# Performance work log

Measured on AMD Instinct MI355X. Metric: run time of the kernel, lower is better.

## Reference

```python
import jax, jax.numpy as jnp
from jax import lax
import numpy as np

NE = 8          # ne_num
IDX_REF = 4     # ne_num // 2
EPS_BN = 1e-5


def conv2d(x, w, b=None, pad=0):
    out = lax.conv_general_dilated(x, w, (1, 1), [(pad, pad), (pad, pad)],
                                   dimension_numbers=('NCHW', 'OIHW', 'NCHW'))
    if b is not None:
        out = out + b[None, :, None, None]
    return out


def bn(x, gamma, beta):
    # training-mode batch norm (biased variance), as nn.BatchNorm2d in train()
    mu = x.mean(axis=(0, 2, 3), keepdims=True)
    var = x.var(axis=(0, 2, 3), keepdims=True)
    xn = (x - mu) * lax.rsqrt(var + EPS_BN)
    return xn * gamma[None, :, None, None] + beta[None, :, None, None]


def gauss_win(sigma):
    # sigma: (B,1). window_size=3 -> bias = [-1, 0, -1]; pop center of 3x3 -> (B,8)
    bias = jnp.array([-1.0, 0.0, -1.0], dtype=sigma.dtype)
    g = jnp.exp(bias[None, :] / (2.0 * sigma ** 2))            # (B,3)
    w1 = g / g.sum(axis=1, keepdims=True)                      # (B,3)
    w2 = (w1[:, :, None] * w1[:, None, :]).reshape(-1, 9)      # (B,9)
    return jnp.concatenate([w2[:, :4], w2[:, 5:]], axis=1)     # (B,8) center removed


def bilinear(img, y, x):
    # img: (B,H,W); y,x: (B,K,H,W) float sample coords; zero padding outside
    B, H, W = img.shape
    y0 = jnp.floor(y); x0 = jnp.floor(x)
    wy1 = y - y0; wy0 = 1.0 - wy1
    wx1 = x - x0; wx0 = 1.0 - wx1
    imgf = img.reshape(B, -1)

    def gather(yi, xi):
        yii = yi.astype(jnp.int32); xii = xi.astype(jnp.int32)
        valid = (yii >= 0) & (yii < H) & (xii >= 0) & (xii < W)
        idx = jnp.clip(yii, 0, H - 1) * W + jnp.clip(xii, 0, W - 1)
        v = jnp.take_along_axis(imgf, idx.reshape(B, -1), axis=1).reshape(idx.shape)
        return jnp.where(valid, v, 0.0)

    return (wy0 * wx0 * gather(y0, x0) + wy0 * wx1 * gather(y0, x0 + 1.0)
            + wy1 * wx0 * gather(y0 + 1.0, x0) + wy1 * wx1 * gather(y0 + 1.0, x0 + 1.0))


def modulated_deform_conv_1x9(fusion, offset, mask):
    # ModulatedDeformConvFunction with weight=ones(1,1,3,3), bias=0, stride=1,
    # pad=1, dilation=1, groups=1, deformable_groups=1.
    # fusion: (B,1,H,W); offset: (B,9,2,H,W) [per-neighbor (dy,dx)]; mask: (B,9,H,W)
    B, _, H, W = fusion.shape
    k = jnp.arange(9)
    py = (k // 3 - 1).astype(fusion.dtype)[None, :, None, None]
    px = (k % 3 - 1).astype(fusion.dtype)[None, :, None, None]
    hh = jnp.arange(H, dtype=fusion.dtype)[None, None, :, None]
    ww = jnp.arange(W, dtype=fusion.dtype)[None, None, None, :]
    y = hh + py + offset[:, :, 0]
    x = ww + px + offset[:, :, 1]
    samp = bilinear(fusion[:, 0], y, x)            # (B,9,H,W)
    return (mask * samp).sum(axis=1, keepdims=True)  # (B,1,H,W)


def _forward(feat, g1_w, g1_g, g1_b, g2_w, g2_g, g2_b, g3_w, g3_bias,
             f1_w, f1_g, f1_b, f2_w, f2_bias,
             s1_w, s1_b, s2_w, s2_b, s3_w, s3_b,
             oa1_w, oa1_g, oa1_b, oa2_w, oa2_g, oa2_b, oa3_w, oa3_bias,
             aff_scale):
    B, _, H, W = feat.shape
    # guid branch (5x5 convs)
    guid = jax.nn.relu(bn(conv2d(feat, g1_w, pad=2), g1_g, g1_b))
    guid = jax.nn.relu(bn(conv2d(guid, g2_w, pad=2), g2_g, g2_b))
    guid = conv2d(guid, g3_w, g3_bias, pad=2)                      # (B,8,H,W)
    # fuse branch
    f = jax.nn.relu(bn(conv2d(feat, f1_w, pad=1), f1_g, f1_b))
    fusion = jnp.tanh(conv2d(f, f2_w, f2_bias, pad=1))             # (B,1,H,W)
    # sigma branch (CAM, detached input)
    fd = lax.stop_gradient(feat)
    p = fd.mean(axis=(2, 3))                                       # (B,32)
    h = jax.nn.celu(p @ s1_w.T + s1_b)
    h = jax.nn.celu(h @ s2_w.T + s2_b)
    sigma = jax.nn.relu(h @ s3_w.T + s3_b) + 0.001                 # (B,1)
    # get_off_aff(guid, sigma, sigma_gamma=0.2, window_size=3)
    oa = jax.nn.relu(bn(conv2d(guid, oa1_w, pad=2), oa1_g, oa1_b))
    oa = jax.nn.relu(bn(conv2d(oa, oa2_w, pad=2), oa2_g, oa2_b))
    oa = conv2d(oa, oa3_w, oa3_bias, pad=2)                        # (B,24,H,W)
    o1, o2, affc = jnp.split(oa, 3, axis=1)                        # each (B,8,H,W)
    off = jnp.concatenate([o1, o2], axis=1).reshape(B, NE, 2, H, W)
    zero_ref = jnp.zeros((B, 1, 2, H, W), dtype=off.dtype)
    offset = jnp.concatenate([off[:, :IDX_REF], zero_ref, off[:, IDX_REF:]], axis=1)  # (B,9,2,H,W)
    gk = gauss_win(sigma + 0.2)                                    # (B,8)
    aff = jnp.tanh(affc) / (aff_scale + 1e-5) + gk[:, :, None, None]
    sa = jnp.abs(aff).sum(axis=1, keepdims=True) + 1e-5
    sa = jnp.maximum(sa, 1.0)
    aff = aff / sa
    aff_ref = 1.0 - aff.sum(axis=1, keepdims=True)
    aff9 = jnp.concatenate([aff[:, :IDX_REF], aff_ref, aff[:, IDX_REF:]], axis=1)  # (B,9,H,W)
    # gauss_filter (times=1) + abs
    gfusion = jnp.abs(modulated_deform_conv_1x9(fusion, offset, aff9))
    return gfusion


def setup_inputs() -> dict:
    key = jax.random.key(0)
    ks = list(jax.random.split(key, 32))
    B, C, H, W = 8, 32, 320, 320
    ne = NE
    d = {}
    d['feat'] = jax.random.normal(ks[0], (B, C, H, W), jnp.float32)

    def wconv(k, o, i, s):
        return jax.random.normal(k, (o, i, s, s), jnp.float32) * (1.0 / np.sqrt(i * s * s))

    def wlin(k, o, i):
        return jax.random.normal(k, (o, i), jnp.float32) * (1.0 / np.sqrt(i))

    # guid: 32->32 (5), 32->8 (5), 8->8 (5, bias)
    d['g1_w'] = wconv(ks[1], C, C, 5); d['g1_g'] = jnp.ones(C) + 0.1 * jax.random.normal(ks[2], (C,)); d['g1_b'] = 0.1 * jax.random.normal(ks[3], (C,))
    d['g2_w'] = wconv(ks[4], ne, C, 5); d['g2_g'] = jnp.ones(ne) + 0.1 * jax.random.normal(ks[5], (ne,)); d['g2_b'] = 0.1 * jax.random.normal(ks[6], (ne,))
    d['g3_w'] = wconv(ks[7], ne, ne, 5); d['g3_bias'] = 0.1 * jax.random.normal(ks[8], (ne,))
    # fuse: 32->32 (3), 32->1 (3, bias)
    d['f1_w'] = wconv(ks[9], C, C, 3); d['f1_g'] = jnp.ones(C) + 0.1 * jax.random.normal(ks[10], (C,)); d['f1_b'] = 0.1 * jax.random.normal(ks[11], (C,))
    d['f2_w'] = wconv(ks[12], 1, C, 3); d['f2_bias'] = 0.1 * jax.random.normal(ks[13], (1,))
    # gen_sigma CAM: 32->16->16->1
    d['s1_w'] = wlin(ks[14], 16, C); d['s1_b'] = 0.1 * jax.random.normal(ks[15], (16,))
    d['s2_w'] = wlin(ks[16], 16, 16); d['s2_b'] = 0.1 * jax.random.normal(ks[17], (16,))
    d['s3_w'] = wlin(ks[18], 1, 16); d['s3_b'] = 0.1 * jax.random.normal(ks[19], (1,))
    # conv_off_aff: 8->8 (5), 8->24 (5), 24->24 (5, bias)
    d['oa1_w'] = wconv(ks[20], ne, ne, 5); d['oa1_g'] = jnp.ones(ne) + 0.1 * jax.random.normal(ks[21], (ne,)); d['oa1_b'] = 0.1 * jax.random.normal(ks[22], (ne,))
    d['oa2_w'] = wconv(ks[23], 3 * ne, ne, 5); d['oa2_g'] = jnp.ones(3 * ne) + 0.1 * jax.random.normal(ks[24], (3 * ne,)); d['oa2_b'] = 0.1 * jax.random.normal(ks[25], (3 * ne,))
    d['oa3_w'] = wconv(ks[26], 3 * ne, 3 * ne, 5); d['oa3_bias'] = 0.1 * jax.random.normal(ks[27], (3 * ne,))
    # aff_scale_const = aff_gamma * ne_num = 0.5 * 8
    d['aff_scale'] = jnp.full((1,), 4.0, jnp.float32)
    return d


def reference(feat, g1_w, g1_g, g1_b, g2_w, g2_g, g2_b, g3_w, g3_bias,
              f1_w, f1_g, f1_b, f2_w, f2_bias,
              s1_w, s1_b, s2_w, s2_b, s3_w, s3_b,
              oa1_w, oa1_g, oa1_b, oa2_w, oa2_g, oa2_b, oa3_w, oa3_bias,
              aff_scale):
    return _forward(feat, g1_w, g1_g, g1_b, g2_w, g2_g, g2_b, g3_w, g3_bias,
                    f1_w, f1_g, f1_b, f2_w, f2_bias,
                    s1_w, s1_b, s2_w, s2_b, s3_w, s3_b,
                    oa1_w, oa1_g, oa1_b, oa2_w, oa2_g, oa2_b, oa3_w, oa3_bias,
                    aff_scale)
```

## Files before the change

### kernel.cpp

```cpp
#include <hip/hip_runtime.h>
#include <hip/hip_bf16.h>
#include <math.h>

#define B_   8
#define H_   320
#define W_   320
#define HW_  (320*320)

typedef __attribute__((ext_vector_type(8))) short bf16x8;
typedef __attribute__((ext_vector_type(4))) short bf16x4s;
typedef __attribute__((ext_vector_type(4))) float f32x4;

__device__ __forceinline__ short f2b(float v){
    __hip_bfloat16 h = __float2bfloat16(v);
    return *(short*)&h;
}
__device__ __forceinline__ float bf2f(short v){
    unsigned u = ((unsigned)(unsigned short)v) << 16;
    return __uint_as_float(u);
}

__global__ void convert_k(const float* __restrict__ in, short* __restrict__ out,
                          float* __restrict__ psum){
    const int b  = blockIdx.y;
    const int px = blockIdx.x*256 + threadIdx.x;
    const float* src = in + (long)b*32*HW_ + px;
    short* dst = out + ((long)b*HW_ + px)*32;
    float f[32];
    short v[32];
    #pragma unroll
    for (int c=0;c<32;++c){ f[c] = src[(long)c*HW_]; v[c] = f2b(f[c]); }
    #pragma unroll
    for (int s=0;s<4;++s)
        *(bf16x8*)(dst + s*8) = *(bf16x8*)(v + s*8);
    #pragma unroll
    for (int c=0;c<32;++c){
        float s = f[c];
        #pragma unroll
        for (int o=1;o<64;o<<=1) s += __shfl_xor(s, o, 64);
        f[c] = s;
    }
    __shared__ float red[4][32];
    const int lane = threadIdx.x & 63, wid = threadIdx.x >> 6;
    if (lane < 32) red[wid][lane] = f[lane];
    __syncthreads();
    if (threadIdx.x < 32)
        atomicAdd(&psum[b*32 + threadIdx.x],
                  red[0][threadIdx.x]+red[1][threadIdx.x]+red[2][threadIdx.x]+red[3][threadIdx.x]);
}

__global__ void repack_k(const float* __restrict__ sf1, const float* __restrict__ sf2,
                         const float* __restrict__ sg1, const float* __restrict__ sg2,
                         const float* __restrict__ sg3, const float* __restrict__ so1,
                         const float* __restrict__ so2, const float* __restrict__ so3,
                         short* __restrict__ dst){
    const int cum[8]  = {9216,13824,39424,52224,55808,59392,66560,92160};
    const int CINs[8] = {32,32,32,32, 8, 8, 8,24};
    const int CIps[8] = {32,32,32,32, 8, 8, 8,32};
    const int COUTs[8]= {32, 1,32, 8, 8, 8,24,24};
    const int MTs[8]  = { 2, 1, 2, 1, 1, 1, 2, 2};
    const int Ks[8]   = { 3, 3, 5, 5, 5, 5, 5, 5};
    int i = blockIdx.x*256 + threadIdx.x;
    if (i >= 92160) return;
    int s = 0;
    while (i >= cum[s]) ++s;
    const int base = s ? cum[s-1] : 0;
    const int il = i - base;
    const float* src = (s==0)?sf1:(s==1)?sf2:(s==2)?sg1:(s==3)?sg2:(s==4)?sg3:(s==5)?so1:(s==6)?so2:so3;
    const int kl   = il & 31;
    const int co_l = (il >> 5) & 15;
    const int rem  = il >> 9;
    const int MT = MTs[s];
    const int mt = rem % MT;
    const int c  = rem / MT;
    const int K = Ks[s];
    int tap, ci;
    if (CIps[s] == 32){ tap = (c % K)*K + (c / K); ci = kl; }
    else              { tap = c*4 + (kl>>3); ci = kl & 7; }
    const int co = mt*16 + co_l;
    float v = 0.f;
    if (co < COUTs[s] && ci < CINs[s] && tap < K*K){
        const int ky = tap / K, kx = tap - ky*K;
        v = src[((co*CINs[s] + ci)*K + ky)*K + kx];
    }
    dst[i] = f2b(v);
}

__device__ __forceinline__
float deform_px(const float* val, const float* __restrict__ fus_b,
                const float* __restrict__ gk_b, float inv_s, int y, int x){
    float aff[8]; float sa = 0.f;
    #pragma unroll
    for (int n=0;n<8;++n){
        float a = tanhf(val[16+n]) * inv_s + gk_b[n];
        aff[n] = a; sa += fabsf(a);
    }
    sa += 1e-5f;
    sa = fmaxf(sa, 1.f);
    const float isa = 1.f/sa;
    float ssum = 0.f;
    #pragma unroll
    for (int n=0;n<8;++n){ aff[n] *= isa; ssum += aff[n]; }
    const float aff_ref = 1.f - ssum;

    float o = 0.f;
    #pragma unroll
    for (int k=0;k<9;++k){
        float dy, dx, m;
        if (k == 4){ dy = 0.f; dx = 0.f; m = aff_ref; }
        else {
            const int n = (k < 4) ? k : k-1;
            dy = val[2*n];
            dx = val[2*n+1];
            m  = aff[n];
        }
        float yy = (float)(y + k/3 - 1) + dy;
        float xx = (float)(x + k%3 - 1) + dx;
        float y0f = floorf(yy), x0f = floorf(xx);
        int   y0 = (int)y0f,    x0i = (int)x0f;
        float wy1 = yy - y0f, wy0 = 1.f - wy1;
        float wx1 = xx - x0f, wx0 = 1.f - wx1;
        float v00 = (y0  >=0 && y0  <H_ && x0i  >=0 && x0i  <W_) ? fus_b[ y0   *W_ + x0i  ] : 0.f;
        float v01 = (y0  >=0 && y0  <H_ && x0i+1>=0 && x0i+1<W_) ? fus_b[ y0   *W_ + x0i+1] : 0.f;
        float v10 = (y0+1>=0 && y0+1<H_ && x0i  >=0 && x0i  <W_) ? fus_b[(y0+1)*W_ + x0i  ] : 0.f;
        float v11 = (y0+1>=0 && y0+1<H_ && x0i+1>=0 && x0i+1<W_) ? fus_b[(y0+1)*W_ + x0i+1] : 0.f;
        o += m * (wy0*(wx0*v00 + wx1*v01) + wy1*(wx0*v10 + wx1*v11));
    }
    return fabsf(o);
}

template<int CIN, int CIp, int COUT, int MT, int K,
         bool IN_BN, bool OUT_STATS, int OUT_MODE, int OCP>
__global__ __launch_bounds__(256, 4)
void mconv_k(const void* __restrict__ inv,
             const float* __restrict__ bn_sum, const float* __restrict__ bn_sq,
             const float* __restrict__ gamma, const float* __restrict__ beta,
             const short* __restrict__ wr, const float* __restrict__ bias,
             void* __restrict__ outv,
             float* __restrict__ osum, float* __restrict__ osq,
             const float* __restrict__ fus, const float* __restrict__ gk,
             const float* __restrict__ aff_scale){
    constexpr int PAD = K/2;
    constexpr int TH  = 8;
    constexpr int LW  = 32 + K - 1;
    constexpr int LH  = TH + K - 1;
    constexpr int SEGS = CIp/8;
    constexpr int PLANE = LH*LW*8 + 8;
    constexpr int NTAPS  = K*K;
    constexpr int NCHUNK = (CIp==32) ? NTAPS : (NTAPS*CIp + 31)/32;
    constexpr int INB  = (CIp==32) ? (SEGS*PLANE*2) : (LH*LW*8*2);
    constexpr int DUMPB = 256*25*4;
    constexpr int LDSB = (OUT_MODE==3 && INB < DUMPB) ? DUMPB : INB;

    __shared__ __align__(16) char ldsraw[LDSB];
    short* lds_in = (short*)ldsraw;
    __shared__ float sc_sh[2][32];
    __shared__ float red[2][4][32];

    const int tid = threadIdx.x;
    const int b   = blockIdx.z;
    const int x0  = blockIdx.x*32, y0 = blockIdx.y*TH;

    const int lane = tid & 63;
    const int wv   = tid >> 6;
    const int pxn  = lane & 15;
    const int quad = lane >> 4;
    const int row0 = 2*wv;

    if (IN_BN){
        if (tid < 32){
            float s = 1.f, sh2 = 0.f;
            if (tid < CIN){
                const float invN = 1.f/(float)(B_*HW_);
                float mu  = bn_sum[tid]*invN;
                float var = bn_sq[tid]*invN - mu*mu;
                s   = gamma[tid] * rsqrtf(var + 1e-5f);
                sh2 = beta[tid] - mu*s;
            }
            sc_sh[0][tid] = s;
            sc_sh[1][tid] = sh2;
        }
        __syncthreads();
    }

    constexpr int KC = (CIp==32) ? K : 1;
    bf16x8 aC[KC][MT];
    bf16x8 aAll[(CIp==8)?NCHUNK:1][MT];

    if constexpr (CIp == 32){
        #pragma unroll
        for (int ky=0; ky<K; ++ky)
            #pragma unroll
            for (int m=0;m<MT;++m)
                aC[ky][m] = *(const bf16x8*)(wr + ((ky*MT + m)*16 + pxn)*32 + quad*8);
    } else {
        #pragma unroll
        for (int c=0;c<NCHUNK;++c)
            #pragma unroll
            for (int m=0;m<MT;++m)
                aAll[c][m] = *(const bf16x8*)(wr + (((c*MT + m)*16 + pxn)*32 + quad*8));
    }

    {
        const short* src = (const short*)inv + (long)b*HW_*CIp;
        constexpr int NU = LH*LW*SEGS;
        constexpr int NIT = (NU + 255)/256;
        bf16x8 vv[NIT];
        int    la[NIT];
        bool   ib[NIT];
        #pragma unroll
        for (int it=0; it<NIT; ++it){
            const int u = tid + it*256;
            bf16x8 v = {0,0,0,0,0,0,0,0};
            bool inb = false;
            int addr = 0;
            if (u < NU){
                const int r   = u / (LW*SEGS);
                const int rem = u - r*(LW*SEGS);
                const int xl  = rem / SEGS;
                const int seg = rem - xl*SEGS;
                const int gy = y0 + r - PAD, gx = x0 + xl - PAD;
                addr = seg*PLANE + (r*LW + xl)*8;
                inb = (gy>=0 && gy<H_ && gx>=0 && gx<W_);
                if (inb)
                    v = *(const bf16x8*)(src + ((long)gy*W_ + gx)*CIp + seg*8);
            }
            vv[it] = v; la[it] = addr; ib[it] = inb;
        }
        __builtin_amdgcn_sched_barrier(0);
        #pragma unroll
        for (int it=0; it<NIT; ++it){
            const int u = tid + it*256;
            if (u < NU){
                bf16x8 v = vv[it];
                if (IN_BN && ib[it]){
                    const int seg = u - (u/SEGS)*SEGS;
                    #pragma unroll
                    for (int j=0;j<8;++j){
                        float f = bf2f(v[j]);
                        f = fmaxf(fmaf(f, sc_sh[0][seg*8+j], sc_sh[1][seg*8+j]), 0.f);
                        v[j] = f2b(f);
                    }
                }
                *(bf16x8*)&lds_in[la[it]] = v;
            }
        }
    }
    __syncthreads();

    const f32x4 zero = {0.f, 0.f, 0.f, 0.f};
    f32x4 acc[2][MT][2];
    #pragma unroll
    for (int rr=0;rr<2;++rr)
        #pragma unroll
        for (int m=0;m<MT;++m){ acc[rr][m][0] = zero; acc[rr][m][1] = zero; }

    if constexpr (CIp == 32){
        const short* bbase = lds_in + quad*PLANE + (row0*LW + pxn)*8;
        #pragma unroll
        for (int kx=0; kx<K; ++kx){
            bf16x8 bw[3][2];
            #pragma unroll
            for (int r=0;r<2;++r)
                #pragma unroll
                for (int n=0;n<2;++n)
                    bw[r][n] = *(const bf16x8*)(bbase + (r*LW + kx + n*16)*8);
            __builtin_amdgcn_sched_barrier(0);
            #pragma unroll
            for (int ky=0; ky<K; ++ky){
                if (ky < K-1){
                    #pragma unroll
                    for (int n=0;n<2;++n)
                        bw[(ky+2)%3][n] = *(const bf16x8*)(bbase + ((ky+2)*LW + kx + n*16)*8);
                }
                __builtin_amdgcn_sched_barrier(0);
                #pragma unroll
                for (int m=0;m<MT;++m){
                    acc[0][m][0] = __builtin_amdgcn_mfma_f32_16x16x32_bf16(aC[ky][m], bw[ky%3][0],     acc[0][m][0], 0,0,0);
                    acc[0][m][1] = __builtin_amdgcn_mfma_f32_16x16x32_bf16(aC[ky][m], bw[ky%3][1],     acc[0][m][1], 0,0,0);
                    acc[1][m][0] = __builtin_amdgcn_mfma_f32_16x16x32_bf16(aC[ky][m], bw[(ky+1)%3][0], acc[1][m][0], 0,0,0);
                    acc[1][m][1] = __builtin_amdgcn_mfma_f32_16x16x32_bf16(aC[ky][m], bw[(ky+1)%3][1], acc[1][m][1], 0,0,0);
                }
                if (kx+1 < K){
                    #pragma unroll
                    for (int m=0;m<MT;++m)
                        aC[ky][m] = *(const bf16x8*)(wr + ((((kx+1)*K+ky)*MT + m)*16 + pxn)*32 + quad*8);
                }
            }
        }
    } else {
        auto bptr = [&](int c, int rr)->const short*{
            const int row = row0 + rr;
            int t = c*4 + quad;
            if (t >= NTAPS) t = 0;
            const int ky = t / K, kx = t - ky*K;
            return lds_in + ((row+ky)*LW + kx + pxn)*8;
        };

        bf16x8 bcp[2][2][2];
        #pragma unroll
        for (int rr=0;rr<2;++rr){
            const short* bp = bptr(0, rr);
            bcp[0][rr][0] = *(const bf16x8*)bp;
            bcp[0][rr][1] = *(const bf16x8*)(bp + 16*8);
        }

        #pragma unroll
        for (int c=0; c<NCHUNK; ++c){
            if (c+1 < NCHUNK){
                #pragma unroll
                for (int rr=0;rr<2;++rr){
                    const short* bpn = bptr(c+1, rr);
                    bcp[(c+1)&1][rr][0] = *(const bf16x8*)bpn;
                    bcp[(c+1)&1][rr][1] = *(const bf16x8*)(bpn + 16*8);
                }
            }
            __builtin_amdgcn_sched_barrier(0);
            #pragma unroll
            for (int m=0;m<MT;++m)
                #pragma unroll
                for (int rr=0;rr<2;++rr){
                    acc[rr][m][0] = __builtin_amdgcn_mfma_f32_16x16x32_bf16(aAll[c][m], bcp[c&1][rr][0], acc[rr][m][0], 0,0,0);
                    acc[rr][m][1] = __builtin_amdgcn_mfma_f32_16x16x32_bf16(aAll[c][m], bcp[c&1][rr][1], acc[rr][m][1], 0,0,0);
                }
        }
    }

    if (OUT_STATS){
        #pragma unroll
        for (int m=0;m<MT;++m){
            #pragma unroll
            for (int r=0;r<4;++r){
                float v  = acc[0][m][0][r] + acc[0][m][1][r]
                         + acc[1][m][0][r] + acc[1][m][1][r];
                float v2 = acc[0][m][0][r]*acc[0][m][0][r] + acc[0][m][1][r]*acc[0][m][1][r]
                         + acc[1][m][0][r]*acc[1][m][0][r] + acc[1][m][1][r]*acc[1][m][1][r];
                #pragma unroll
                for (int o=1;o<16;o<<=1){
                    v  += __shfl_xor(v,  o, 64);
                    v2 += __shfl_xor(v2, o, 64);
                }
                if (pxn == 0){
                    red[0][wv][m*16 + quad*4 + r] = v;
                    red[1][wv][m*16 + quad*4 + r] = v2;
                }
            }
        }
        __syncthreads();
        if (tid < MT*16 && tid < COUT){
            atomicAdd(&osum[tid], red[0][0][tid]+red[0][1][tid]+red[0][2][tid]+red[0][3][tid]);
            atomicAdd(&osq[tid],  red[1][0][tid]+red[1][1][tid]+red[1][2][tid]+red[1][3][tid]);
        }
    }

    if (OUT_MODE == 3){
        float* out = (float*)outv;
        __syncthreads();
        float* dumpf = (float*)ldsraw;
        #pragma unroll
        for (int rr=0;rr<2;++rr){
            const int row = row0 + rr;
            #pragma unroll
            for (int m=0;m<MT;++m){
                if (m*16 + quad*4 < 24){
                    #pragma unroll
                    for (int n=0;n<2;++n)
                        #pragma unroll
                        for (int r=0;r<4;++r)
                            dumpf[(row*32 + n*16 + pxn)*25 + (m*16 + quad*4 + r)] = acc[rr][m][n][r];
                }
            }
        }
        __syncthreads();
        {
            float val[24];
            #pragma unroll
            for (int c2=0;c2<24;++c2) val[c2] = dumpf[tid*25 + c2] + bias[c2];
            const int yy = y0 + (tid>>5), xx = x0 + (tid&31);
            const float inv_s = 1.f/(aff_scale[0] + 1e-5f);
            out[(long)b*HW_ + yy*W_ + xx] =
                deform_px(val, fus + (long)b*HW_, gk + b*8, inv_s, yy, xx);
        }
    } else if (OUT_MODE == 2){
        float* out = (float*)outv;
        #pragma unroll
        for (int rr=0;rr<2;++rr){
            const int y = y0 + row0 + rr;
            #pragma unroll
            for (int m=0;m<MT;++m){
                #pragma unroll
                for (int r=0;r<4;++r){
                    const int co = m*16 + quad*4 + r;
                    if (co < COUT){
                        float* op = out + (((long)b*COUT + co)*H_ + y)*W_ + x0;
                        #pragma unroll
                        for (int n=0;n<2;++n)
                            op[n*16 + pxn] = tanhf(acc[rr][m][n][r] + bias[co]);
                    }
                }
            }
        }
    } else {
        short* o = (short*)outv;
        #pragma unroll
        for (int rr=0;rr<2;++rr){
            const int y = y0 + row0 + rr;
            #pragma unroll
            for (int m=0;m<MT;++m){
                const int co0 = m*16 + quad*4;
                if (co0 < OCP){
                    #pragma unroll
                    for (int n=0;n<2;++n){
                        bf16x4s pk;
                        #pragma unroll
                        for (int r=0;r<4;++r){
                            float f = acc[rr][m][n][r];
                            if (OUT_MODE == 1) f += bias[co0+r];
                            pk[r] = f2b(f);
                        }
                        const long px = ((long)b*H_ + y)*W_ + x0 + n*16 + pxn;
                        *(bf16x4s*)(o + px*OCP + co0) = pk;
                    }
                }
            }
        }
    }
}

__global__ void sigma_k(const float* __restrict__ p,
                        const float* s1w, const float* s1b,
                        const float* s2w, const float* s2b,
                        const float* s3w, const float* s3b,
                        float* __restrict__ gk){
    const int b = threadIdx.x;
    if (b >= B_) return;
    float pb[32];
    for (int j=0;j<32;++j) pb[j] = p[b*32+j] * (1.f/(float)HW_);
    float h1[16], h2[16];
    for (int i=0;i<16;++i){
        float t = s1b[i];
        for (int j=0;j<32;++j) t = fmaf(pb[j], s1w[i*32+j], t);
        h1[i] = t > 0.f ? t : expm1f(t);
    }
    for (int i=0;i<16;++i){
        float t = s2b[i];
        for (int j=0;j<16;++j) t = fmaf(h1[j], s2w[i*16+j], t);
        h2[i] = t > 0.f ? t : expm1f(t);
    }
    float t = s3b[0];
    for (int j=0;j<16;++j) t = fmaf(h2[j], s3w[j], t);
    float sigma = fmaxf(t, 0.f) + 0.001f;
    float sg = sigma + 0.2f;
    float e = expf(-1.f/(2.f*sg*sg));
    float inv = 1.f/(2.f*e + 1.f);
    float a = e*inv, c = inv;
    float* g = gk + b*8;
    g[0]=a*a; g[1]=a*c; g[2]=a*a; g[3]=c*a; g[4]=c*a; g[5]=a*a; g[6]=a*c; g[7]=a*a;
}

extern "C" void kernel_launch(void* const* d_in, const int* in_sizes, int n_in,
                              void* d_out, int out_size, void* d_ws, size_t ws_size,
                              hipStream_t stream){
    const float* feat    = (const float*)d_in[0];
    const float* g1_w    = (const float*)d_in[1];
    const float* g1_g    = (const float*)d_in[2];
    const float* g1_b    = (const float*)d_in[3];
    const float* g2_w    = (const float*)d_in[4];
    const float* g2_g    = (const float*)d_in[5];
    const float* g2_b    = (const float*)d_in[6];
    const float* g3_w    = (const float*)d_in[7];
    const float* g3_bias = (const float*)d_in[8];
    const float* f1_w    = (const float*)d_in[9];
    const float* f1_g    = (const float*)d_in[10];
    const float* f1_b    = (const float*)d_in[11];
    const float* f2_w    = (const float*)d_in[12];
    const float* f2_bias = (const float*)d_in[13];
    const float* s1w     = (const float*)d_in[14];
    const float* s1b     = (const float*)d_in[15];
    const float* s2w     = (const float*)d_in[16];
    const float* s2b     = (const float*)d_in[17];
    const float* s3w     = (const float*)d_in[18];
    const float* s3b     = (const float*)d_in[19];
    const float* oa1_w   = (const float*)d_in[20];
    const float* oa1_g   = (const float*)d_in[21];
    const float* oa1_b   = (const float*)d_in[22];
    const float* oa2_w   = (const float*)d_in[23];
    const float* oa2_g   = (const float*)d_in[24];
    const float* oa2_b   = (const float*)d_in[25];
    const float* oa3_w   = (const float*)d_in[26];
    const float* oa3_bias= (const float*)d_in[27];
    const float* aff_scale=(const float*)d_in[28];
    float* out = (float*)d_out;

    char* ws = (char*)d_ws;
    short* FEAT = (short*)(ws + 0L);
    short* A1   = (short*)(ws + 52428800L);
    short* A2   = (short*)(ws + 104857600L);
    short* GUID = (short*)(ws + 117964800L);
    float* FUS  = (float*)(ws + 131072000L);
    float* SM   = (float*)(ws + 134348800L);
    short* OA2  = A1;

    float* sum = SM;
    float* sq  = SM + 320;
    float* p   = SM + 640;
    float* gk  = SM + 896;
    short* WBs = (short*)(SM + 960);
    short* w_f1 = WBs + 0;
    short* w_f2 = WBs + 9216;
    short* w_g1 = WBs + 13824;
    short* w_g2 = WBs + 39424;
    short* w_g3 = WBs + 52224;
    short* w_o1 = WBs + 55808;
    short* w_o2 = WBs + 59392;
    short* w_o3 = WBs + 66560;

    hipMemsetAsync(sum, 0, 896*sizeof(float), stream);

    repack_k<<<dim3(360), dim3(256), 0, stream>>>(
        f1_w, f2_w, g1_w, g2_w, g3_w, oa1_w, oa2_w, oa3_w, WBs);
    convert_k<<<dim3(HW_/256, B_), dim3(256), 0, stream>>>(feat, FEAT, p);

    sigma_k<<<dim3(1), dim3(64), 0, stream>>>(p, s1w, s1b, s2w, s2b, s3w, s3b, gk);

    const dim3 cgrid(10, 40, 8), cblk(256);
    #define MCONV(CIN,CIp,COUT,MT,K,IBN,OST,OM,OCP) \
        mconv_k<CIN,CIp,COUT,MT,K,IBN,OST,OM,OCP><<<cgrid,cblk,0,stream>>>

    MCONV(32,32,32,2,3,false,true ,0,32)(FEAT, nullptr, nullptr, nullptr, nullptr,
        w_f1, nullptr, A1, sum+0*64, sq+0*64, nullptr, nullptr, nullptr);
    MCONV(32,32, 1,1,3,true ,false,2, 0)(A1, sum+0*64, sq+0*64, f1_g, f1_b,
        w_f2, f2_bias, FUS, nullptr, nullptr, nullptr, nullptr, nullptr);

    MCONV(32,32,32,2,5,false,true ,0,32)(FEAT, nullptr, nullptr, nullptr, nullptr,
        w_g1, nullptr, A1, sum+1*64, sq+1*64, nullptr, nullptr, nullptr);
    MCONV(32,32, 8,1,5,true ,true ,0, 8)(A1, sum+1*64, sq+1*64, g1_g, g1_b,
        w_g2, nullptr, A2, sum+2*64, sq+2*64, nullptr, nullptr, nullptr);
    MCONV( 8, 8, 8,1,5,true ,false,1, 8)(A2, sum+2*64, sq+2*64, g2_g, g2_b,
        w_g3, g3_bias, GUID, nullptr, nullptr, nullptr, nullptr, nullptr);

    MCONV( 8, 8, 8,1,5,false,true ,0, 8)(GUID, nullptr, nullptr, nullptr, nullptr,
        w_o1, nullptr, A2, sum+3*64, sq+3*64, nullptr, nullptr, nullptr);
    MCONV( 8, 8,24,2,5,true ,true ,0,32)(A2, sum+3*64, sq+3*64, oa1_g, oa1_b,
        w_o2, nullptr, OA2, sum+4*64, sq+4*64, nullptr, nullptr, nullptr);
    MCONV(24,32,24,2,5,true ,false,3, 0)(OA2, sum+4*64, sq+4*64, oa2_g, oa2_b,
        w_o3, oa3_bias, out, nullptr, nullptr, FUS, gk, aff_scale);
    #undef MCONV
}
```

Measured before the change: 596.8 us.

## Fuse f1 and g1 convolutions into one kernel sharing the staged input tile

Adds a kernel that loads the 32-channel feature tile (with a 2-pixel halo) into LDS once, then runs both the 3x3 f1 conv and the 5x5 g1 conv from it with MFMA, writing two outputs and their BN statistics. This removes one full read of FEAT and one kernel launch. It needs a separate workspace buffer for the g1 output and only runs when the workspace is large enough, falling back to the old path otherwise. The LDS footprint and register pressure are higher, which could reduce occupancy.

```diff
diff --git a/kernel.cpp b/kernel.cpp
--- a/kernel.cpp
+++ b/kernel.cpp
@@ -427,6 +427,188 @@
     }
 }
 
+template<int KK, int OFF>
+__device__ __forceinline__
+void conv_core32(const short* __restrict__ lds_in, const short* __restrict__ wr,
+                 int row0, int pxn, int quad, f32x4 acc[2][2][2]){
+    constexpr int LW = 36;
+    constexpr int PLANE = 12*36*8 + 8;
+    const short* bbase = lds_in + quad*PLANE + ((row0+OFF)*LW + OFF + pxn)*8;
+    bf16x8 aC[KK][2];
+    #pragma unroll
+    for (int ky=0; ky<KK; ++ky)
+        #pragma unroll
+        for (int m=0;m<2;++m)
+            aC[ky][m] = *(const bf16x8*)(wr + ((ky*2 + m)*16 + pxn)*32 + quad*8);
+    #pragma unroll
+    for (int kx=0; kx<KK; ++kx){
+        bf16x8 bw[3][2];
+        #pragma unroll
+        for (int r=0;r<2;++r)
+            #pragma unroll
+            for (int n=0;n<2;++n)
+                bw[r][n] = *(const bf16x8*)(bbase + (r*LW + kx + n*16)*8);
+        __builtin_amdgcn_sched_barrier(0);
+        #pragma unroll
+        for (int ky=0; ky<KK; ++ky){
+            if (ky < KK-1){
+                #pragma unroll
+                for (int n=0;n<2;++n)
+                    bw[(ky+2)%3][n] = *(const bf16x8*)(bbase + ((ky+2)*LW + kx + n*16)*8);
+            }
+            __builtin_amdgcn_sched_barrier(0);
+            #pragma unroll
+            for (int m=0;m<2;++m){
+                acc[0][m][0] = __builtin_amdgcn_mfma_f32_16x16x32_bf16(aC[ky][m], bw[ky%3][0],     acc[0][m][0], 0,0,0);
+                acc[0][m][1] = __builtin_amdgcn_mfma_f32_16x16x32_bf16(aC[ky][m], bw[ky%3][1],     acc[0][m][1], 0,0,0);
+                acc[1][m][0] = __builtin_amdgcn_mfma_f32_16x16x32_bf16(aC[ky][m], bw[(ky+1)%3][0], acc[1][m][0], 0,0,0);
+                acc[1][m][1] = __builtin_amdgcn_mfma_f32_16x16x32_bf16(aC[ky][m], bw[(ky+1)%3][1], acc[1][m][1], 0,0,0);
+            }
+            if (kx+1 < KK){
+                #pragma unroll
+                for (int m=0;m<2;++m)
+                    aC[ky][m] = *(const bf16x8*)(wr + ((((kx+1)*KK+ky)*2 + m)*16 + pxn)*32 + quad*8);
+            }
+        }
+    }
+}
+
+__global__ __launch_bounds__(256, 4)
+void mconv_fg_k(const short* __restrict__ feat,
+                const short* __restrict__ wf, const short* __restrict__ wg,
+                short* __restrict__ f1o, short* __restrict__ g1o,
+                float* __restrict__ sum0, float* __restrict__ sq0,
+                float* __restrict__ sum1, float* __restrict__ sq1){
+    constexpr int PAD = 2, LW = 36, LH = 12, SEGS = 4;
+    constexpr int PLANE = LH*LW*8 + 8;
+
+    __shared__ __align__(16) char ldsraw[SEGS*PLANE*2];
+    short* lds_in = (short*)ldsraw;
+    __shared__ float red[2][4][32];
+
+    const int tid = threadIdx.x;
+    const int b   = blockIdx.z;
+    const int x0  = blockIdx.x*32, y0 = blockIdx.y*8;
+
+    const int lane = tid & 63;
+    const int wv   = tid >> 6;
+    const int pxn  = lane & 15;
+    const int quad = lane >> 4;
+    const int row0 = 2*wv;
+
+    {
+        const short* src = feat + (long)b*HW_*32;
+        constexpr int NU = LH*LW*SEGS;
+        constexpr int NIT = (NU + 255)/256;
+        bf16x8 vv[NIT];
+        int    la[NIT];
+        #pragma unroll
+        for (int it=0; it<NIT; ++it){
+            const int u = tid + it*256;
+            bf16x8 v = {0,0,0,0,0,0,0,0};
+            int addr = 0;
+            if (u < NU){
+                const int r   = u / (LW*SEGS);
+                const int rem = u - r*(LW*SEGS);
+                const int xl  = rem / SEGS;
+                const int seg = rem - xl*SEGS;
+                const int gy = y0 + r - PAD, gx = x0 + xl - PAD;
+                addr = seg*PLANE + (r*LW + xl)*8;
+                if (gy>=0 && gy<H_ && gx>=0 && gx<W_)
+                    v = *(const bf16x8*)(src + ((long)gy*W_ + gx)*32 + seg*8);
+            }
+            vv[it] = v; la[it] = addr;
+        }
+        __builtin_amdgcn_sched_barrier(0);
+        #pragma unroll
+        for (int it=0; it<NIT; ++it){
+            if (tid + it*256 < NU)
+                *(bf16x8*)&lds_in[la[it]] = vv[it];
+        }
+    }
+    __syncthreads();
+
+    const f32x4 zero = {0.f, 0.f, 0.f, 0.f};
+    f32x4 acc[2][2][2];
+
+    #pragma unroll
+    for (int rr=0;rr<2;++rr)
+        #pragma unroll
+        for (int m=0;m<2;++m){ acc[rr][m][0] = zero; acc[rr][m][1] = zero; }
+    conv_core32<3,1>(lds_in, wf, row0, pxn, quad, acc);
+    #pragma unroll
+    for (int m=0;m<2;++m)
+        #pragma unroll
+        for (int r=0;r<4;++r){
+            float v  = acc[0][m][0][r] + acc[0][m][1][r] + acc[1][m][0][r] + acc[1][m][1][r];
+            float v2 = acc[0][m][0][r]*acc[0][m][0][r] + acc[0][m][1][r]*acc[0][m][1][r]
+                     + acc[1][m][0][r]*acc[1][m][0][r] + acc[1][m][1][r]*acc[1][m][1][r];
+            #pragma unroll
+            for (int o=1;o<16;o<<=1){ v += __shfl_xor(v, o, 64); v2 += __shfl_xor(v2, o, 64); }
+            if (pxn == 0){ red[0][wv][m*16+quad*4+r] = v; red[1][wv][m*16+quad*4+r] = v2; }
+        }
+    __syncthreads();
+    if (tid < 32){
+        atomicAdd(&sum0[tid], red[0][0][tid]+red[0][1][tid]+red[0][2][tid]+red[0][3][tid]);
+        atomicAdd(&sq0[tid],  red[1][0][tid]+red[1][1][tid]+red[1][2][tid]+red[1][3][tid]);
+    }
+    #pragma unroll
+    for (int rr=0;rr<2;++rr){
+        const int y = y0 + row0 + rr;
+        #pragma unroll
+        for (int m=0;m<2;++m){
+            const int co0 = m*16 + quad*4;
+            #pragma unroll
+            for (int n=0;n<2;++n){
+                bf16x4s pk;
+                #pragma unroll
+                for (int r=0;r<4;++r) pk[r] = f2b(acc[rr][m][n][r]);
+                const long px = ((long)b*H_ + y)*W_ + x0 + n*16 + pxn;
+                *(bf16x4s*)(f1o + px*32 + co0) = pk;
+            }
+        }
+    }
+    __syncthreads();
+
+    #pragma unroll
+    for (int rr=0;rr<2;++rr)
+        #pragma unroll
+        for (int m=0;m<2;++m){ acc[rr][m][0] = zero; acc[rr][m][1] = zero; }
+    conv_core32<5,0>(lds_in, wg, row0, pxn, quad, acc);
+    #pragma unroll
+    for (int m=0;m<2;++m)
+        #pragma unroll
+        for (int r=0;r<4;++r){
+            float v  = acc[0][m][0][r] + acc[0][m][1][r] + acc[1][m][0][r] + acc[1][m][1][r];
+            float v2 = acc[0][m][0][r]*acc[0][m][0][r] + acc[0][m][1][r]*acc[0][m][1][r]
+                     + acc[1][m][0][r]*acc[1][m][0][r] + acc[1][m][1][r]*acc[1][m][1][r];
+            #pragma unroll
+            for (int o=1;o<16;o<<=1){ v += __shfl_xor(v, o, 64); v2 += __shfl_xor(v2, o, 64); }
+            if (pxn == 0){ red[0][wv][m*16+quad*4+r] = v; red[1][wv][m*16+quad*4+r] = v2; }
+        }
+    __syncthreads();
+    if (tid < 32){
+        atomicAdd(&sum1[tid], red[0][0][tid]+red[0][1][tid]+red[0][2][tid]+red[0][3][tid]);
+        atomicAdd(&sq1[tid],  red[1][0][tid]+red[1][1][tid]+red[1][2][tid]+red[1][3][tid]);
+    }
+    #pragma unroll
+    for (int rr=0;rr<2;++rr){
+        const int y = y0 + row0 + rr;
+        #pragma unroll
+        for (int m=0;m<2;++m){
+            const int co0 = m*16 + quad*4;
+            #pragma unroll
+            for (int n=0;n<2;++n){
+                bf16x4s pk;
+                #pragma unroll
+                for (int r=0;r<4;++r) pk[r] = f2b(acc[rr][m][n][r]);
+                const long px = ((long)b*H_ + y)*W_ + x0 + n*16 + pxn;
+                *(bf16x4s*)(g1o + px*32 + co0) = pk;
+            }
+        }
+    }
+}
+
 __global__ void sigma_k(const float* __restrict__ p,
                         const float* s1w, const float* s1b,
                         const float* s2w, const float* s2b,
@@ -500,6 +682,8 @@
     float* FUS  = (float*)(ws + 131072000L);
     float* SM   = (float*)(ws + 134348800L);
     short* OA2  = A1;
+    short* G1O  = (short*)(ws + 135266304L);
+    const bool merged = (ws_size >= 135266304UL + 52428800UL);
 
     float* sum = SM;
     float* sq  = SM + 320;
@@ -527,14 +711,24 @@
     #define MCONV(CIN,CIp,COUT,MT,K,IBN,OST,OM,OCP) \
         mconv_k<CIN,CIp,COUT,MT,K,IBN,OST,OM,OCP><<<cgrid,cblk,0,stream>>>
 
-    MCONV(32,32,32,2,3,false,true ,0,32)(FEAT, nullptr, nullptr, nullptr, nullptr,
-        w_f1, nullptr, A1, sum+0*64, sq+0*64, nullptr, nullptr, nullptr);
-    MCONV(32,32, 1,1,3,true ,false,2, 0)(A1, sum+0*64, sq+0*64, f1_g, f1_b,
-        w_f2, f2_bias, FUS, nullptr, nullptr, nullptr, nullptr, nullptr);
-
-    MCONV(32,32,32,2,5,false,true ,0,32)(FEAT, nullptr, nullptr, nullptr, nullptr,
-        w_g1, nullptr, A1, sum+1*64, sq+1*64, nullptr, nullptr, nullptr);
-    MCONV(32,32, 8,1,5,true ,true ,0, 8)(A1, sum+1*64, sq+1*64, g1_g, g1_b,
+    const short* G1SRC;
+    if (merged){
+        mconv_fg_k<<<cgrid, cblk, 0, stream>>>(FEAT, w_f1, w_g1, A1, G1O,
+                                               sum+0*64, sq+0*64, sum+1*64, sq+1*64);
+        MCONV(32,32, 1,1,3,true ,false,2, 0)(A1, sum+0*64, sq+0*64, f1_g, f1_b,
+            w_f2, f2_bias, FUS, nullptr, nullptr, nullptr, nullptr, nullptr);
+        G1SRC = G1O;
+    } else {
+        MCONV(32,32,32,2,3,false,true ,0,32)(FEAT, nullptr, nullptr, nullptr, nullptr,
+            w_f1, nullptr, A1, sum+0*64, sq+0*64, nullptr, nullptr, nullptr);
+        MCONV(32,32, 1,1,3,true ,false,2, 0)(A1, sum+0*64, sq+0*64, f1_g, f1_b,
+            w_f2, f2_bias, FUS, nullptr, nullptr, nullptr, nullptr, nullptr);
+        MCONV(32,32,32,2,5,false,true ,0,32)(FEAT, nullptr, nullptr, nullptr, nullptr,
+            w_g1, nullptr, A1, sum+1*64, sq+1*64, nullptr, nullptr, nullptr);
+        G1SRC = A1;
+    }
+
+    MCONV(32,32, 8,1,5,true ,true ,0, 8)(G1SRC, sum+1*64, sq+1*64, g1_g, g1_b,
         w_g2, nullptr, A2, sum+2*64, sq+2*64, nullptr, nullptr, nullptr);
     MCONV( 8, 8, 8,1,5,true ,false,1, 8)(A2, sum+2*64, sq+2*64, g2_g, g2_b,
         w_g3, g3_bias, GUID, nullptr, nullptr, nullptr, nullptr, nullptr);
```

Result: faster. 567.4 us (median of 2 runs) (-4.9%).
